# Performance work log

Measured on AMD Instinct MI355X. Metric: run time of the kernel, lower is better.

Reference implementation:

```python
import jax, jax.numpy as jnp
import numpy as np

B, T, C, H = 1, 2048, 1024, 16
HD = C // H           # 64
TOPK = 64
RAMP = 32
MAX_SPAN = 2048
NEG_MAX = jnp.finfo(jnp.float32).max


def setup_inputs() -> dict:
    key = jax.random.key(0)
    k0, k1, k2, k3, k4 = jax.random.split(key, 5)
    x = jax.random.normal(k0, (B, T, C), jnp.float32)
    w_attn = jax.random.normal(k1, (3 * C, C), jnp.float32) * 0.02
    w_proj = jax.random.normal(k2, (C, C), jnp.float32) * 0.02
    w_gate = jax.random.normal(k3, (C, C), jnp.float32) * 0.02
    span_params = jax.random.uniform(k4, (H,), jnp.float32)
    pos = jnp.arange(T, dtype=jnp.int64) if jax.config.jax_enable_x64 else jnp.arange(T, dtype=jnp.int32)
    return {"x": x, "w_attn": w_attn, "w_proj": w_proj, "w_gate": w_gate,
            "span_params": span_params, "pos": pos}


def _rotate_half(u):
    u1, u2 = jnp.split(u, 2, axis=-1)
    return jnp.concatenate([-u2, u1], axis=-1)


def _rope(q, k):
    t = q.shape[-2]
    inv_freq = 1.0 / (10000.0 ** (jnp.arange(0, HD, 2, dtype=jnp.float32) / HD))
    freqs = jnp.arange(t, dtype=jnp.float32)[:, None] * inv_freq[None, :]  # [T, HD/2]
    emb = jnp.concatenate([freqs, freqs], axis=-1)                          # [T, HD]
    cos = jnp.cos(emb)[None, None]
    sin = jnp.sin(emb)[None, None]
    q = q * cos + _rotate_half(q * sin)
    k = k * cos + _rotate_half(k * sin)
    return q, k


def reference(x, w_attn, w_proj, w_gate, span_params, pos):
    qkv = x @ w_attn.T                                   # [B,T,3C]
    q, k, v = jnp.split(qkv, 3, axis=-1)
    q = q.reshape(B, T, H, HD).transpose(0, 2, 1, 3)     # [B,H,T,HD]
    k = k.reshape(B, T, H, HD).transpose(0, 2, 1, 3)
    v = v.reshape(B, T, H, HD).transpose(0, 2, 1, 3)
    q, k = _rope(q, k)

    att = jnp.einsum('bhqd,bhkd->bhqk', q, k) / jnp.sqrt(jnp.float32(HD))
    i = jnp.arange(T)
    causal = i[:, None] >= i[None, :]                    # [T,T]
    att = jnp.where(causal[None, None], att, -jnp.inf)

    # sparse top-k with straight-through softmax
    top_vals = jax.lax.top_k(att, TOPK)[0]               # [B,H,T,K]
    thresh = top_vals[..., -1:]
    keep = (att >= thresh) & (att > -NEG_MAX)
    att_topk = jnp.where(keep, att, -NEG_MAX)
    topk_attn = jax.nn.softmax(att_topk, axis=-1)
    soft_attn = jax.nn.softmax(att, axis=-1)
    att = jax.lax.stop_gradient(topk_attn) + soft_attn - jax.lax.stop_gradient(soft_attn)

    # adaptive span soft mask + renormalize
    spans = MAX_SPAN * jnp.clip(span_params, 0.0, 1.0)   # [H]
    dist = jnp.abs(i[:, None] - i[None, :]).astype(jnp.float32)  # [T,T]
    soft_mask = jnp.clip((RAMP + spans[:, None, None] - dist[None]) / RAMP, 0.0, 1.0)  # [H,T,T]
    att = att * soft_mask[None]
    att = att / (att.sum(-1, keepdims=True) + 1e-8)

    y = jnp.einsum('bhqk,bhkd->bhqd', att, v)            # [B,H,T,HD]
    y = y.transpose(0, 2, 1, 3).reshape(B, T, C)
    gate = jax.nn.silu(x @ w_gate.T)
    y = y * gate
    y = y @ w_proj.T
    return y
```

## Files before the change

kernel.cpp:

```cpp
#include <hip/hip_runtime.h>
#include <math.h>

#define T_DIM 2048
#define C_DIM 1024
#define H_DIM 16
#define HD 64
#define TOPK_K 64
#define QTILE 8
#define LCAP 128

typedef __attribute__((ext_vector_type(8))) __bf16 bf16x8;
typedef __attribute__((ext_vector_type(4))) float f32x4;

__device__ __forceinline__ unsigned short bf16rn(float x) {
  unsigned u = __float_as_uint(x);
  return (unsigned short)((u + 0x7FFFu + ((u >> 16) & 1u)) >> 16);
}
__device__ __forceinline__ unsigned f2u(float f) {
  unsigned u = __float_as_uint(f);
  return (u & 0x80000000u) ? ~u : (u | 0x80000000u);
}
__device__ __forceinline__ float u2f(unsigned u) {
  unsigned v = (u & 0x80000000u) ? (u & 0x7FFFFFFFu) : ~u;
  return __uint_as_float(v);
}
__device__ __forceinline__ bf16x8 ld_frag(const uint4* p) {
  uint4 u = *p;
  return __builtin_bit_cast(bf16x8, u);
}
#define PAD_KEY 0x007FFFFFu

__global__ __launch_bounds__(256) void convert_all_kernel(
    const float* __restrict__ x, const float* __restrict__ wa,
    const float* __restrict__ wg, const float* __restrict__ wp,
    unsigned short* __restrict__ xh, unsigned short* __restrict__ xl,
    unsigned short* __restrict__ wqgh, unsigned short* __restrict__ wqgl,
    unsigned short* __restrict__ wph, unsigned short* __restrict__ wpl,
    float2* __restrict__ tab)
{
  const int tid = blockIdx.x * 256 + threadIdx.x;
  const int k8 = tid & 127, r = tid >> 7;
  if (r >= 7168) {
    const int e = ((r - 7168) << 7) | k8;
    const int t = e >> 5, d = e & 31;
    double invf = exp(-(double)d * (log(10000.0) / 32.0));
    double ang = (double)t * invf;
    tab[e] = make_float2((float)cos(ang), (float)sin(ang));
    return;
  }
  const float* src;
  unsigned short *Dh, *Dl;
  int srow, drow;
  if (r < 2048)      { src = x;  Dh = xh;   Dl = xl;   srow = r;        drow = r; }
  else if (r < 5120) { src = wa; Dh = wqgh; Dl = wqgl; srow = r - 2048; drow = r - 2048; }
  else if (r < 6144) { src = wg; Dh = wqgh; Dl = wqgl; srow = r - 5120; drow = r - 2048; }
  else               { src = wp; Dh = wph;  Dl = wpl;  srow = r - 6144; drow = r - 6144; }
  const float* s = src + ((size_t)srow << 10) + (k8 << 3);
  float4 a = *(const float4*)s;
  float4 b = *(const float4*)(s + 4);
  float xs[8] = {a.x, a.y, a.z, a.w, b.x, b.y, b.z, b.w};
  unsigned hi[8], lo[8];
#pragma unroll
  for (int jj = 0; jj < 8; ++jj) {
    unsigned short hb = bf16rn(xs[jj]);
    hi[jj] = hb;
    lo[jj] = bf16rn(xs[jj] - __uint_as_float((unsigned)hb << 16));
  }
  const int t16 = drow >> 4, rr = drow & 15, kc = k8 >> 2, kq = k8 & 3;
  const size_t elem = (((size_t)(t16 * 32 + kc)) * 64 + ((kq << 4) | rr)) * 8;
  uint4 vh, vl;
  vh.x = hi[0] | (hi[1] << 16); vh.y = hi[2] | (hi[3] << 16);
  vh.z = hi[4] | (hi[5] << 16); vh.w = hi[6] | (hi[7] << 16);
  vl.x = lo[0] | (lo[1] << 16); vl.y = lo[2] | (lo[3] << 16);
  vl.z = lo[4] | (lo[5] << 16); vl.w = lo[6] | (lo[7] << 16);
  *(uint4*)(Dh + elem) = vh;
  *(uint4*)(Dl + elem) = vl;
}

__device__ __forceinline__ void gld_lds16(const unsigned short* g, unsigned short* l) {
  __builtin_amdgcn_global_load_lds(
      (const __attribute__((address_space(1))) unsigned int*)g,
      (__attribute__((address_space(3))) unsigned int*)l, 16, 0, 0);
}

__global__ __launch_bounds__(512, 4) void mgemm_qkvg_kernel(
    const unsigned short* __restrict__ Ah, const unsigned short* __restrict__ Al,
    const unsigned short* __restrict__ Bh, const unsigned short* __restrict__ Bl,
    float* __restrict__ Cq, float* __restrict__ Ck, float* __restrict__ Cv,
    float* __restrict__ Cg)
{
  __shared__ __align__(16) unsigned short As[2 * 8 * 512];
  __shared__ __align__(16) unsigned short Bs[2 * 8 * 512];
  const int tid = threadIdx.x, lane = tid & 63, w = tid >> 6;
  const int mt0 = blockIdx.y << 3;
  const int nt0 = blockIdx.x << 3;

  f32x4 acc[8];
#pragma unroll
  for (int j = 0; j < 8; ++j) acc[j] = (f32x4){0.f, 0.f, 0.f, 0.f};

  for (int kc = 0; kc < 32; ++kc) {
#pragma unroll
    for (int li = 0; li < 4; ++li) {
      const int gi = (w << 2) + li;
      const int isB = gi >= 16;
      const int gb = gi & 15;
      const int t  = gb & 7;
      const int hl = gb >> 3;
      const unsigned short* gbase = isB ? (hl ? Bl : Bh) : (hl ? Al : Ah);
      const int tg = (isB ? nt0 : mt0) + t;
      const unsigned short* g = gbase + (((size_t)(tg * 32 + kc) << 6) + lane) * 8;
      unsigned short* l = (isB ? Bs : As) + hl * 4096 + t * 512;
      gld_lds16(g, l);
    }
    __syncthreads();
    bf16x8 ah = *(const bf16x8*)&As[w * 512 + lane * 8];
    bf16x8 al = *(const bf16x8*)&As[4096 + w * 512 + lane * 8];
#pragma unroll
    for (int j = 0; j < 8; ++j) {
      bf16x8 bh = *(const bf16x8*)&Bs[j * 512 + lane * 8];
      bf16x8 bl = *(const bf16x8*)&Bs[4096 + j * 512 + lane * 8];
      acc[j] = __builtin_amdgcn_mfma_f32_16x16x32_bf16(ah, bh, acc[j], 0, 0, 0);
      acc[j] = __builtin_amdgcn_mfma_f32_16x16x32_bf16(ah, bl, acc[j], 0, 0, 0);
      acc[j] = __builtin_amdgcn_mfma_f32_16x16x32_bf16(al, bh, acc[j], 0, 0, 0);
    }
    __syncthreads();
  }

  const int col = lane & 15, quad = lane >> 4;
  const int mbase = (blockIdx.y << 7) + (w << 4);
#pragma unroll
  for (int j = 0; j < 8; ++j) {
    const int ncol = (blockIdx.x << 7) + (j << 4);
    const int which = ncol >> 10;
    if (which < 3) {
      const int h = (ncol & 1023) >> 6;
      float* dst = (which == 0) ? Cq : (which == 1) ? Ck : Cv;
      float* base = dst + (((size_t)h * T_DIM) << 6) + (ncol & 63) + col;
#pragma unroll
      for (int reg = 0; reg < 4; ++reg) {
        const int m = mbase + quad * 4 + reg;
        base[(size_t)m << 6] = acc[j][reg];
      }
    } else {
      const int cb = (ncol & 1023) + col;
#pragma unroll
      for (int reg = 0; reg < 4; ++reg) {
        const int m = mbase + quad * 4 + reg;
        float vv = acc[j][reg];
        Cg[((size_t)m << 10) + cb] = vv / (1.f + expf(-vv));
      }
    }
  }
}

__global__ __launch_bounds__(256, 4) void mgemm_proj_kernel(
    const unsigned short* __restrict__ Ah, const unsigned short* __restrict__ Al,
    const unsigned short* __restrict__ Bh, const unsigned short* __restrict__ Bl,
    float* __restrict__ P0, float* __restrict__ P1)
{
  __shared__ __align__(16) unsigned short As[2 * 4 * 512];
  __shared__ __align__(16) unsigned short Bs[2 * 8 * 512];
  const int tid = threadIdx.x, lane = tid & 63, w = tid >> 6;
  const int mt0 = blockIdx.y << 2;
  const int nt0 = blockIdx.x << 3;
  const int kc0 = blockIdx.z << 4;
  float* Cout = blockIdx.z ? P1 : P0;

  f32x4 acc[8];
#pragma unroll
  for (int j = 0; j < 8; ++j) acc[j] = (f32x4){0.f, 0.f, 0.f, 0.f};

  for (int kc = kc0; kc < kc0 + 16; ++kc) {
#pragma unroll
    for (int li = 0; li < 6; ++li) {
      const int gi = w * 6 + li;
      const int isB = gi >= 8;
      const int t  = isB ? ((gi - 8) & 7) : (gi & 3);
      const int hl = isB ? ((gi - 8) >> 3) : (gi >> 2);
      const unsigned short* gbase = isB ? (hl ? Bl : Bh) : (hl ? Al : Ah);
      const int tg = (isB ? nt0 : mt0) + t;
      const unsigned short* g = gbase + (((size_t)(tg * 32 + kc) << 6) + lane) * 8;
      unsigned short* l = isB ? (Bs + hl * 4096 + t * 512) : (As + hl * 2048 + t * 512);
      gld_lds16(g, l);
    }
    __syncthreads();
    bf16x8 ah = *(const bf16x8*)&As[w * 512 + lane * 8];
    bf16x8 al = *(const bf16x8*)&As[2048 + w * 512 + lane * 8];
#pragma unroll
    for (int j = 0; j < 8; ++j) {
      bf16x8 bh = *(const bf16x8*)&Bs[j * 512 + lane * 8];
      bf16x8 bl = *(const bf16x8*)&Bs[4096 + j * 512 + lane * 8];
      acc[j] = __builtin_amdgcn_mfma_f32_16x16x32_bf16(ah, bh, acc[j], 0, 0, 0);
      acc[j] = __builtin_amdgcn_mfma_f32_16x16x32_bf16(ah, bl, acc[j], 0, 0, 0);
      acc[j] = __builtin_amdgcn_mfma_f32_16x16x32_bf16(al, bh, acc[j], 0, 0, 0);
    }
    __syncthreads();
  }

  const int col = lane & 15, quad = lane >> 4;
  const int mbase = (blockIdx.y << 6) + (w << 4);
  const int nbase = blockIdx.x << 7;
#pragma unroll
  for (int j = 0; j < 8; ++j)
#pragma unroll
    for (int reg = 0; reg < 4; ++reg) {
      const int m = mbase + quad * 4 + reg;
      Cout[((size_t)m << 10) + nbase + (j << 4) + col] = acc[j][reg];
    }
}

__global__ __launch_bounds__(256) void add2_kernel(
    const float* __restrict__ P0, const float* __restrict__ P1,
    float* __restrict__ out)
{
  const int i = (blockIdx.x * 256 + threadIdx.x) << 2;
  float4 a = *(const float4*)(P0 + i);
  float4 b = *(const float4*)(P1 + i);
  float4 o = {a.x + b.x, a.y + b.y, a.z + b.z, a.w + b.w};
  *(float4*)(out + i) = o;
}

__global__ __launch_bounds__(64) void prep_frag_kernel(
    float* __restrict__ qb, float* __restrict__ kb,
    const float2* __restrict__ tab)
{
  float* buf = blockIdx.z ? kb : qb;
  const int lane = threadIdx.x;
  const int t16 = blockIdx.x, h = blockIdx.y;
  const int nr = lane & 15, quad = lane >> 4;
  const int t = (t16 << 4) + nr;
  const float* row = buf + ((size_t)(h * T_DIM + t) << 6);
  const int d0 = quad << 3;
  float4 a0 = *(const float4*)(row + d0);
  float4 a1 = *(const float4*)(row + d0 + 4);
  float4 b0 = *(const float4*)(row + 32 + d0);
  float4 b1 = *(const float4*)(row + 32 + d0 + 4);
  float x0[8] = {a0.x, a0.y, a0.z, a0.w, a1.x, a1.y, a1.z, a1.w};
  float x1[8] = {b0.x, b0.y, b0.z, b0.w, b1.x, b1.y, b1.z, b1.w};
  const float2* tb = tab + t * 32 + d0;
  unsigned short h0[8], l0[8], h1[8], l1[8];
#pragma unroll
  for (int jj = 0; jj < 8; ++jj) {
    float2 cs2 = tb[jj];
    float o0 = fmaf(x0[jj], cs2.x, -x1[jj] * cs2.y);
    float o1 = fmaf(x1[jj], cs2.x, x0[jj] * cs2.y);
    unsigned short hb = bf16rn(o0);
    h0[jj] = hb;
    l0[jj] = bf16rn(o0 - __uint_as_float((unsigned)hb << 16));
    hb = bf16rn(o1);
    h1[jj] = hb;
    l1[jj] = bf16rn(o1 - __uint_as_float((unsigned)hb << 16));
  }
  char* base = (char*)buf + (((size_t)(h * 128 + t16)) << 12);
  uint4 v;
  v.x = (unsigned)h0[0] | ((unsigned)h0[1] << 16);
  v.y = (unsigned)h0[2] | ((unsigned)h0[3] << 16);
  v.z = (unsigned)h0[4] | ((unsigned)h0[5] << 16);
  v.w = (unsigned)h0[6] | ((unsigned)h0[7] << 16);
  ((uint4*)base)[lane] = v;
  v.x = (unsigned)h1[0] | ((unsigned)h1[1] << 16);
  v.y = (unsigned)h1[2] | ((unsigned)h1[3] << 16);
  v.z = (unsigned)h1[4] | ((unsigned)h1[5] << 16);
  v.w = (unsigned)h1[6] | ((unsigned)h1[7] << 16);
  ((uint4*)(base + 1024))[lane] = v;
  v.x = (unsigned)l0[0] | ((unsigned)l0[1] << 16);
  v.y = (unsigned)l0[2] | ((unsigned)l0[3] << 16);
  v.z = (unsigned)l0[4] | ((unsigned)l0[5] << 16);
  v.w = (unsigned)l0[6] | ((unsigned)l0[7] << 16);
  ((uint4*)(base + 2048))[lane] = v;
  v.x = (unsigned)l1[0] | ((unsigned)l1[1] << 16);
  v.y = (unsigned)l1[2] | ((unsigned)l1[3] << 16);
  v.z = (unsigned)l1[4] | ((unsigned)l1[5] << 16);
  v.w = (unsigned)l1[6] | ((unsigned)l1[7] << 16);
  ((uint4*)(base + 3072))[lane] = v;
}

__global__ __launch_bounds__(512, 6) void attn_kernel(
    const float* __restrict__ qfrag, const float* __restrict__ kfrag,
    const float* __restrict__ v, const float* __restrict__ span_params,
    const float* __restrict__ gate,
    unsigned short* __restrict__ Yh, unsigned short* __restrict__ Yl)
{
  __shared__ __align__(16) char smem[QTILE * 1024 * 4];
  float* sBase = (float*)smem;
  unsigned* histB = (unsigned*)smem;
  int* listJB = (int*)(smem + 8192);
  unsigned* listUB = (unsigned*)(smem + 12288);

  const int tid = threadIdx.x;
  const int lane = tid & 63;
  const int w = tid >> 6;
  const int bx = gridDim.x - 1 - blockIdx.x;
  const int q0 = bx << 3;
  const int h = blockIdx.y;
  const int qi = q0 + w;
  const int n = qi + 1;
  const float* vh = v + (((size_t)h * T_DIM) << 6);
  const int col = lane & 15, quad = lane >> 4;

  const int qt16 = bx >> 1;
  const int rlo = (bx & 1) << 3;
  const uint4* qf = (const uint4*)((const char*)qfrag + (((size_t)(h * 128 + qt16)) << 12));
  bf16x8 Ah0 = ld_frag(qf + lane);
  bf16x8 Ah1 = ld_frag(qf + 64 + lane);
  bf16x8 Al0 = ld_frag(qf + 128 + lane);
  bf16x8 Al1 = ld_frag(qf + 192 + lane);

  unsigned uk[32];

#pragma unroll
  for (int ph = 0; ph < 2; ++ph) {
    const int tlo = ph << 6;
    const int thi = (qt16 < tlo + 63) ? qt16 : (tlo + 63);
    int tf = tlo + w;
    if (tf <= thi) {
      const uint4* kf = (const uint4*)((const char*)kfrag + (((size_t)(h * 128 + tf)) << 12));
      bf16x8 nBh0 = ld_frag(kf + lane);
      bf16x8 nBh1 = ld_frag(kf + 64 + lane);
      bf16x8 nBl0 = ld_frag(kf + 128 + lane);
      bf16x8 nBl1 = ld_frag(kf + 192 + lane);
      for (; tf <= thi; tf += 8) {
        const bf16x8 Bh0 = nBh0, Bh1 = nBh1, Bl0 = nBl0, Bl1 = nBl1;
        const int tn = (tf + 8 <= thi) ? (tf + 8) : tf;
        const uint4* kfn = (const uint4*)((const char*)kfrag + (((size_t)(h * 128 + tn)) << 12));
        nBh0 = ld_frag(kfn + lane);
        nBh1 = ld_frag(kfn + 64 + lane);
        nBl0 = ld_frag(kfn + 128 + lane);
        nBl1 = ld_frag(kfn + 192 + lane);
        f32x4 acc = {0.f, 0.f, 0.f, 0.f};
        acc = __builtin_amdgcn_mfma_f32_16x16x32_bf16(Ah0, Bh0, acc, 0, 0, 0);
        acc = __builtin_amdgcn_mfma_f32_16x16x32_bf16(Ah0, Bl0, acc, 0, 0, 0);
        acc = __builtin_amdgcn_mfma_f32_16x16x32_bf16(Al0, Bh0, acc, 0, 0, 0);
        acc = __builtin_amdgcn_mfma_f32_16x16x32_bf16(Ah1, Bh1, acc, 0, 0, 0);
        acc = __builtin_amdgcn_mfma_f32_16x16x32_bf16(Ah1, Bl1, acc, 0, 0, 0);
        acc = __builtin_amdgcn_mfma_f32_16x16x32_bf16(Al1, Bh1, acc, 0, 0, 0);
        const int jcol = (tf << 4) + col;
#pragma unroll
        for (int r = 0; r < 4; ++r) {
          const int row8 = (quad << 2) + r - rlo;
          if ((unsigned)row8 < 8u && jcol <= q0 + row8)
            sBase[row8 * 1024 + ((jcol & 1023) ^ (((row8 >> 2) & 1) << 4))] = acc[r];
        }
      }
    }
    __syncthreads();
#pragma unroll
    for (int cc = 0; cc < 2; ++cc) {
      const int c = (ph << 1) + cc;
      if ((c << 9) < n) {
#pragma unroll
        for (int i = 0; i < 8; ++i) {
          const int j = (((c << 3) + i) << 6) + lane;
          uk[(c << 3) + i] = (j < n)
              ? f2u(sBase[w * 1024 + ((j & 1023) ^ (((w >> 2) & 1) << 4))]) : PAD_KEY;
        }
      } else {
#pragma unroll
        for (int i = 0; i < 8; ++i) uk[(c << 3) + i] = PAD_KEY;
      }
    }
    __syncthreads();
  }

  unsigned* hist = histB + (w << 8);
  int* listJ = listJB + (w << 7);
  unsigned* listU = listUB + (w << 7);
  const float span = 2048.f * fminf(fmaxf(span_params[h], 0.f), 1.f);

  unsigned umax = 0;
#pragma unroll
  for (int i = 0; i < 32; ++i) umax = max(umax, uk[i]);
#pragma unroll
  for (int off = 32; off > 0; off >>= 1)
    umax = max(umax, (unsigned)__shfl_xor((int)umax, off, 64));
  const float mraw = u2f(umax);

  unsigned thresh_u = 0;
  if (n > TOPK_K) {
    unsigned want = TOPK_K;
    const unsigned bmax = umax >> 24;
    unsigned long long c01 = 0;
#pragma unroll
    for (int c = 0; c < 4; ++c) {
      if ((c << 9) < n) {
#pragma unroll
        for (int i = 0; i < 8; ++i) {
          const unsigned u = uk[(c << 3) + i];
          const unsigned d = bmax - (u >> 24);
          if (u > PAD_KEY && d < 4u) c01 += 1ull << (d << 4);
        }
      }
    }
#pragma unroll
    for (int off = 32; off > 0; off >>= 1)
      c01 += __shfl_xor(c01, off, 64);
    unsigned cnt8[8];
    cnt8[0] = (unsigned)c01 & 0xFFFFu;
    cnt8[1] = ((unsigned)c01) >> 16;
    cnt8[2] = (unsigned)(c01 >> 32) & 0xFFFFu;
    cnt8[3] = (unsigned)(c01 >> 48);
    int m = -1;
    unsigned cumBefore = 0;
    bool exact = false;
    unsigned cum = 0;
#pragma unroll
    for (int b = 0; b < 4; ++b) {
      if (m < 0 && cum + cnt8[b] >= want) {
        m = b; cumBefore = cum; exact = (cum + cnt8[b] == want);
      }
      cum += cnt8[b];
    }
    if (m < 0) {
      unsigned long long c23 = 0;
#pragma unroll
      for (int c = 0; c < 4; ++c) {
        if ((c << 9) < n) {
#pragma unroll
          for (int i = 0; i < 8; ++i) {
            const unsigned u = uk[(c << 3) + i];
            const unsigned d = bmax - (u >> 24) - 4u;
            if (u > PAD_KEY && d < 4u) c23 += 1ull << (d << 4);
          }
        }
      }
#pragma unroll
      for (int off = 32; off > 0; off >>= 1)
        c23 += __shfl_xor(c23, off, 64);
      cnt8[4] = (unsigned)c23 & 0xFFFFu;
      cnt8[5] = ((unsigned)c23) >> 16;
      cnt8[6] = (unsigned)(c23 >> 32) & 0xFFFFu;
      cnt8[7] = (unsigned)(c23 >> 48);
#pragma unroll
      for (int b = 4; b < 8; ++b) {
        if (m < 0 && cum + cnt8[b] >= want) {
          m = b; cumBefore = cum; exact = (cum + cnt8[b] == want);
        }
        cum += cnt8[b];
      }
    }
    unsigned prefix;
    int shift0;
    if (m >= 0) { prefix = (bmax - (unsigned)m) << 24; want -= cumBefore; shift0 = 16; }
    else        { prefix = 0; shift0 = 24; }
    if (m >= 0 && exact) {
      thresh_u = prefix;
    } else {
      for (int shift = shift0; shift >= 0; shift -= 8) {
        uint4 z4 = {0u, 0u, 0u, 0u};
        *(uint4*)&hist[lane << 2] = z4;
        __threadfence_block();
        const unsigned pm = (shift == 24) ? 0u : (0xFFFFFFFFu << (shift + 8));
#pragma unroll
        for (int c = 0; c < 4; ++c) {
          if ((c << 9) < n) {
#pragma unroll
            for (int i = 0; i < 8; ++i) {
              const unsigned u = uk[(c << 3) + i];
              if (u > PAD_KEY && (u & pm) == prefix)
                atomicAdd(&hist[(u >> shift) & 255u], 1u);
            }
          }
        }
        __threadfence_block();
        uint4 hv = *(const uint4*)&hist[lane << 2];
        unsigned loc = hv.x + hv.y + hv.z + hv.w;
        unsigned suf = loc;
#pragma unroll
        for (int off = 1; off < 64; off <<= 1) {
          unsigned t = __shfl_down(suf, off, 64);
          suf += (lane + off < 64) ? t : 0u;
        }
        unsigned sufE = suf - loc;
        unsigned S3 = sufE + hv.w;
        unsigned S2 = S3 + hv.z;
        unsigned S1 = S2 + hv.y;
        unsigned S0 = S1 + hv.x;
        const unsigned wt = want;
        int found = 0;
        unsigned pk = 0;
        if (S0 >= wt && S1 < wt)
          { found = 1; pk = ((unsigned)(4*lane+0) << 16) | ((S0 == wt) ? 0x8000u : 0u) | (wt - S1); }
        if (S1 >= wt && S2 < wt)
          { found = 1; pk = ((unsigned)(4*lane+1) << 16) | ((S1 == wt) ? 0x8000u : 0u) | (wt - S2); }
        if (S2 >= wt && S3 < wt)
          { found = 1; pk = ((unsigned)(4*lane+2) << 16) | ((S2 == wt) ? 0x8000u : 0u) | (wt - S3); }
        if (S3 >= wt && sufE < wt)
          { found = 1; pk = ((unsigned)(4*lane+3) << 16) | ((S3 == wt) ? 0x8000u : 0u) | (wt - sufE); }
        unsigned long long mk = __ballot(found);
        int src = __ffsll(mk) - 1;
        pk = __shfl(pk, src, 64);
        prefix |= (pk >> 16) << shift;
        want = pk & 0x7FFFu;
        if (pk & 0x8000u) break;
      }
      thresh_u = prefix;
    }
  }

  int cnt_run = 0;
#pragma unroll
  for (int c = 0; c < 4; ++c) {
    if ((c << 9) < n) {
#pragma unroll
      for (int i = 0; i < 8; ++i) {
        const int j = (((c << 3) + i) << 6) + lane;
        const unsigned u = uk[(c << 3) + i];
        const bool keep = (u >= thresh_u) && (u > PAD_KEY);
        unsigned long long mb = __ballot(keep);
        if (keep) {
          int pos = cnt_run + (int)__popcll(mb & ((1ull << lane) - 1ull));
          if (pos < LCAP) { listJ[pos] = j; listU[pos] = u; }
        }
        cnt_run += (int)__popcll(mb);
      }
    }
  }
  const int cnt = min(cnt_run, LCAP);
  __threadfence_block();

  float Zl = 0.f, Ul = 0.f;
  for (int e = lane; e < cnt; e += 64) {
    const unsigned u = listU[e];
    const int j = listJ[e];
    const float wv = __expf((u2f(u) - mraw) * 0.125f);
    const float dist = (float)(qi - j);
    const float msk = fminf(fmaxf((32.f + span - dist) * (1.f / 32.f), 0.f), 1.f);
    const float wm = wv * msk;
    Zl += wv;
    Ul += wm;
    listU[e] = __float_as_uint(wm);
  }
#pragma unroll
  for (int off = 32; off > 0; off >>= 1) {
    Zl += __shfl_xor(Zl, off, 64);
    Ul += __shfl_xor(Ul, off, 64);
  }
  const float scale = 1.f / (Ul + 1e-8f * Zl);
  __threadfence_block();

  const int g = lane >> 4;
  const int d4 = col << 2;
  float4 acc4 = {0.f, 0.f, 0.f, 0.f};
  for (int e0 = 0; e0 < cnt; e0 += 16) {
    int j0 = 0, j1 = 0, j2 = 0, j3 = 0;
    float wm0 = 0.f, wm1 = 0.f, wm2 = 0.f, wm3 = 0.f;
    {
      const int e = e0 + g;
      if (e < cnt) { j0 = listJ[e]; wm0 = __uint_as_float(listU[e]); }
    }
    {
      const int e = e0 + 4 + g;
      if (e < cnt) { j1 = listJ[e]; wm1 = __uint_as_float(listU[e]); }
    }
    {
      const int e = e0 + 8 + g;
      if (e < cnt) { j2 = listJ[e]; wm2 = __uint_as_float(listU[e]); }
    }
    {
      const int e = e0 + 12 + g;
      if (e < cnt) { j3 = listJ[e]; wm3 = __uint_as_float(listU[e]); }
    }
    const float4 v0 = *(const float4*)(vh + ((size_t)j0 << 6) + d4);
    const float4 v1 = *(const float4*)(vh + ((size_t)j1 << 6) + d4);
    const float4 v2 = *(const float4*)(vh + ((size_t)j2 << 6) + d4);
    const float4 v3 = *(const float4*)(vh + ((size_t)j3 << 6) + d4);
    acc4.x = fmaf(wm0, v0.x, acc4.x);
    acc4.y = fmaf(wm0, v0.y, acc4.y);
    acc4.z = fmaf(wm0, v0.z, acc4.z);
    acc4.w = fmaf(wm0, v0.w, acc4.w);
    acc4.x = fmaf(wm1, v1.x, acc4.x);
    acc4.y = fmaf(wm1, v1.y, acc4.y);
    acc4.z = fmaf(wm1, v1.z, acc4.z);
    acc4.w = fmaf(wm1, v1.w, acc4.w);
    acc4.x = fmaf(wm2, v2.x, acc4.x);
    acc4.y = fmaf(wm2, v2.y, acc4.y);
    acc4.z = fmaf(wm2, v2.z, acc4.z);
    acc4.w = fmaf(wm2, v2.w, acc4.w);
    acc4.x = fmaf(wm3, v3.x, acc4.x);
    acc4.y = fmaf(wm3, v3.y, acc4.y);
    acc4.z = fmaf(wm3, v3.z, acc4.z);
    acc4.w = fmaf(wm3, v3.w, acc4.w);
  }
#pragma unroll
  for (int off = 16; off <= 32; off <<= 1) {
    acc4.x += __shfl_xor(acc4.x, off, 64);
    acc4.y += __shfl_xor(acc4.y, off, 64);
    acc4.z += __shfl_xor(acc4.z, off, 64);
    acc4.w += __shfl_xor(acc4.w, off, 64);
  }
  if (g == 0) {
    const int c0 = (h << 6) + d4;
    const float4 gv = *(const float4*)(gate + ((size_t)qi << 10) + c0);
    float p[4] = {acc4.x * scale * gv.x, acc4.y * scale * gv.y,
                  acc4.z * scale * gv.z, acc4.w * scale * gv.w};
    unsigned short ph[4], pl[4];
#pragma unroll
    for (int jj = 0; jj < 4; ++jj) {
      unsigned short hb = bf16rn(p[jj]);
      ph[jj] = hb;
      pl[jj] = bf16rn(p[jj] - __uint_as_float((unsigned)hb << 16));
    }
    const int k8 = c0 >> 3;
    const int t16 = qi >> 4, rr = qi & 15, kc = k8 >> 2, kq = k8 & 3;
    const size_t elem = (((size_t)(t16 * 32 + kc)) * 64 + ((kq << 4) | rr)) * 8 + (d4 & 7);
    ushort4 vh4 = {ph[0], ph[1], ph[2], ph[3]};
    ushort4 vl4 = {pl[0], pl[1], pl[2], pl[3]};
    *(ushort4*)(Yh + elem) = vh4;
    *(ushort4*)(Yl + elem) = vl4;
  }
}

extern "C" void kernel_launch(void* const* d_in, const int* in_sizes, int n_in,
                              void* d_out, int out_size, void* d_ws, size_t ws_size,
                              hipStream_t stream) {
  (void)in_sizes; (void)n_in; (void)out_size; (void)ws_size;
  const float* x           = (const float*)d_in[0];
  const float* w_attn      = (const float*)d_in[1];
  const float* w_proj      = (const float*)d_in[2];
  const float* w_gate      = (const float*)d_in[3];
  const float* span_params = (const float*)d_in[4];
  float* out = (float*)d_out;

  char* ws = (char*)d_ws;
  const size_t MB = 1024 * 1024;
  float* q     = (float*)(ws);
  float* k     = (float*)(ws + 8 * MB);
  float* v     = (float*)(ws + 16 * MB);
  float* gate  = (float*)(ws + 24 * MB);
  unsigned short* xf_h  = (unsigned short*)(ws + 40 * MB);
  unsigned short* xf_l  = (unsigned short*)(ws + 44 * MB);
  unsigned short* wqg_h = (unsigned short*)(ws + 48 * MB);
  unsigned short* wqg_l = (unsigned short*)(ws + 56 * MB);
  unsigned short* wfp_h = (unsigned short*)(ws + 64 * MB);
  unsigned short* wfp_l = (unsigned short*)(ws + 66 * MB);
  unsigned short* ygf_h = (unsigned short*)(ws + 68 * MB);
  unsigned short* ygf_l = (unsigned short*)(ws + 72 * MB);
  float2* rope_tab = (float2*)(ws + 76 * MB);
  float* P0 = q;
  float* P1 = k;

  convert_all_kernel<<<3840, 256, 0, stream>>>(
      x, w_attn, w_gate, w_proj, xf_h, xf_l, wqg_h, wqg_l, wfp_h, wfp_l, rope_tab);
  mgemm_qkvg_kernel<<<dim3(32, 16), 512, 0, stream>>>(
      xf_h, xf_l, wqg_h, wqg_l, q, k, v, gate);
  prep_frag_kernel<<<dim3(T_DIM / 16, H_DIM, 2), 64, 0, stream>>>(q, k, rope_tab);
  attn_kernel<<<dim3(T_DIM / QTILE, H_DIM), 512, 0, stream>>>(
      q, k, v, span_params, gate, ygf_h, ygf_l);
  mgemm_proj_kernel<<<dim3(8, 32, 2), 256, 0, stream>>>(
      ygf_h, ygf_l, wfp_h, wfp_l, P0, P1);
  add2_kernel<<<(T_DIM * C_DIM) / 1024, 256, 0, stream>>>(P0, P1, out);
}
```

Before: 281.2 us.

## Fuse RoPE fragment prep into QKV GEMM epilogue and split proj GEMM 4-way

The RoPE rotation and bf16 hi/lo fragment packing for Q and K now run in the QKV GEMM epilogue, staged through LDS, which removes the separate prep_frag kernel and its extra fp32 round trip through global memory. The output projection GEMM is split four ways along K instead of two, doubling the block count for better CU occupancy. That costs more partial-sum traffic in a four-input reduction kernel and a larger LDS footprint in the QKV GEMM.

```diff
diff --git a/kernel.cpp b/kernel.cpp
--- a/kernel.cpp
+++ b/kernel.cpp
@@ -87,10 +87,11 @@
     const unsigned short* __restrict__ Ah, const unsigned short* __restrict__ Al,
     const unsigned short* __restrict__ Bh, const unsigned short* __restrict__ Bl,
     float* __restrict__ Cq, float* __restrict__ Ck, float* __restrict__ Cv,
-    float* __restrict__ Cg)
+    float* __restrict__ Cg, const float2* __restrict__ tab)
 {
-  __shared__ __align__(16) unsigned short As[2 * 8 * 512];
-  __shared__ __align__(16) unsigned short Bs[2 * 8 * 512];
+  __shared__ __align__(16) char smemAll[34816];
+  unsigned short* As = (unsigned short*)smemAll;
+  unsigned short* Bs = (unsigned short*)(smemAll + 16384);
   const int tid = threadIdx.x, lane = tid & 63, w = tid >> 6;
   const int mt0 = blockIdx.y << 3;
   const int nt0 = blockIdx.x << 3;
@@ -128,27 +129,85 @@
   }
 
   const int col = lane & 15, quad = lane >> 4;
-  const int mbase = (blockIdx.y << 7) + (w << 4);
-#pragma unroll
-  for (int j = 0; j < 8; ++j) {
-    const int ncol = (blockIdx.x << 7) + (j << 4);
-    const int which = ncol >> 10;
-    if (which < 3) {
-      const int h = (ncol & 1023) >> 6;
-      float* dst = (which == 0) ? Cq : (which == 1) ? Ck : Cv;
-      float* base = dst + (((size_t)h * T_DIM) << 6) + (ncol & 63) + col;
-#pragma unroll
-      for (int reg = 0; reg < 4; ++reg) {
-        const int m = mbase + quad * 4 + reg;
-        base[(size_t)m << 6] = acc[j][reg];
-      }
-    } else {
-      const int cb = (ncol & 1023) + col;
-#pragma unroll
-      for (int reg = 0; reg < 4; ++reg) {
-        const int m = mbase + quad * 4 + reg;
-        float vv = acc[j][reg];
-        Cg[((size_t)m << 10) + cb] = vv / (1.f + expf(-vv));
+  const int bxx = blockIdx.x;
+  if (bxx < 16) {
+    float* W = (float*)smemAll + w * (16 * 66);
+    float* qkbuf = (bxx < 8) ? Cq : Ck;
+    const int hb = (bxx & 7) << 1;
+    const int t16 = (blockIdx.y << 3) + w;
+    const int t = (t16 << 4) + col;
+    const float2* tb = tab + t * 32 + (quad << 3);
+#pragma unroll
+    for (int jh = 0; jh < 2; ++jh) {
+#pragma unroll
+      for (int j2 = 0; j2 < 4; ++j2)
+#pragma unroll
+        for (int reg = 0; reg < 4; ++reg)
+          W[(quad * 4 + reg) * 66 + (j2 << 4) + col] = acc[(jh << 2) + j2][reg];
+      const float* rowp = W + col * 66;
+      float x0[8], x1[8];
+#pragma unroll
+      for (int jj = 0; jj < 8; ++jj) {
+        x0[jj] = rowp[(quad << 3) + jj];
+        x1[jj] = rowp[32 + (quad << 3) + jj];
+      }
+      unsigned short h0[8], l0[8], h1[8], l1[8];
+#pragma unroll
+      for (int jj = 0; jj < 8; ++jj) {
+        float2 cs2 = tb[jj];
+        float o0 = fmaf(x0[jj], cs2.x, -x1[jj] * cs2.y);
+        float o1 = fmaf(x1[jj], cs2.x, x0[jj] * cs2.y);
+        unsigned short hbb = bf16rn(o0);
+        h0[jj] = hbb;
+        l0[jj] = bf16rn(o0 - __uint_as_float((unsigned)hbb << 16));
+        hbb = bf16rn(o1);
+        h1[jj] = hbb;
+        l1[jj] = bf16rn(o1 - __uint_as_float((unsigned)hbb << 16));
+      }
+      char* base = (char*)qkbuf + (((size_t)((hb + jh) * 128 + t16)) << 12);
+      uint4 v;
+      v.x = (unsigned)h0[0] | ((unsigned)h0[1] << 16);
+      v.y = (unsigned)h0[2] | ((unsigned)h0[3] << 16);
+      v.z = (unsigned)h0[4] | ((unsigned)h0[5] << 16);
+      v.w = (unsigned)h0[6] | ((unsigned)h0[7] << 16);
+      ((uint4*)base)[lane] = v;
+      v.x = (unsigned)h1[0] | ((unsigned)h1[1] << 16);
+      v.y = (unsigned)h1[2] | ((unsigned)h1[3] << 16);
+      v.z = (unsigned)h1[4] | ((unsigned)h1[5] << 16);
+      v.w = (unsigned)h1[6] | ((unsigned)h1[7] << 16);
+      ((uint4*)(base + 1024))[lane] = v;
+      v.x = (unsigned)l0[0] | ((unsigned)l0[1] << 16);
+      v.y = (unsigned)l0[2] | ((unsigned)l0[3] << 16);
+      v.z = (unsigned)l0[4] | ((unsigned)l0[5] << 16);
+      v.w = (unsigned)l0[6] | ((unsigned)l0[7] << 16);
+      ((uint4*)(base + 2048))[lane] = v;
+      v.x = (unsigned)l1[0] | ((unsigned)l1[1] << 16);
+      v.y = (unsigned)l1[2] | ((unsigned)l1[3] << 16);
+      v.z = (unsigned)l1[4] | ((unsigned)l1[5] << 16);
+      v.w = (unsigned)l1[6] | ((unsigned)l1[7] << 16);
+      ((uint4*)(base + 3072))[lane] = v;
+    }
+  } else {
+    const int mbase = (blockIdx.y << 7) + (w << 4);
+#pragma unroll
+    for (int j = 0; j < 8; ++j) {
+      const int ncol = (bxx << 7) + (j << 4);
+      if (bxx < 24) {
+        const int h = (ncol & 1023) >> 6;
+        float* base = Cv + (((size_t)h * T_DIM) << 6) + (ncol & 63) + col;
+#pragma unroll
+        for (int reg = 0; reg < 4; ++reg) {
+          const int m = mbase + quad * 4 + reg;
+          base[(size_t)m << 6] = acc[j][reg];
+        }
+      } else {
+        const int cb = (ncol & 1023) + col;
+#pragma unroll
+        for (int reg = 0; reg < 4; ++reg) {
+          const int m = mbase + quad * 4 + reg;
+          float vv = acc[j][reg];
+          Cg[((size_t)m << 10) + cb] = vv / (1.f + expf(-vv));
+        }
       }
     }
   }
@@ -157,21 +216,23 @@
 __global__ __launch_bounds__(256, 4) void mgemm_proj_kernel(
     const unsigned short* __restrict__ Ah, const unsigned short* __restrict__ Al,
     const unsigned short* __restrict__ Bh, const unsigned short* __restrict__ Bl,
-    float* __restrict__ P0, float* __restrict__ P1)
+    float* __restrict__ P0, float* __restrict__ P1,
+    float* __restrict__ P2, float* __restrict__ P3)
 {
   __shared__ __align__(16) unsigned short As[2 * 4 * 512];
   __shared__ __align__(16) unsigned short Bs[2 * 8 * 512];
   const int tid = threadIdx.x, lane = tid & 63, w = tid >> 6;
   const int mt0 = blockIdx.y << 2;
   const int nt0 = blockIdx.x << 3;
-  const int kc0 = blockIdx.z << 4;
-  float* Cout = blockIdx.z ? P1 : P0;
+  const int kc0 = blockIdx.z << 3;
+  float* Cout = (blockIdx.z == 0) ? P0 : (blockIdx.z == 1) ? P1
+              : (blockIdx.z == 2) ? P2 : P3;
 
   f32x4 acc[8];
 #pragma unroll
   for (int j = 0; j < 8; ++j) acc[j] = (f32x4){0.f, 0.f, 0.f, 0.f};
 
-  for (int kc = kc0; kc < kc0 + 16; ++kc) {
+  for (int kc = kc0; kc < kc0 + 8; ++kc) {
 #pragma unroll
     for (int li = 0; li < 6; ++li) {
       const int gi = w * 6 + li;
@@ -210,70 +271,19 @@
     }
 }
 
-__global__ __launch_bounds__(256) void add2_kernel(
+__global__ __launch_bounds__(256) void add4_kernel(
     const float* __restrict__ P0, const float* __restrict__ P1,
+    const float* __restrict__ P2, const float* __restrict__ P3,
     float* __restrict__ out)
 {
   const int i = (blockIdx.x * 256 + threadIdx.x) << 2;
   float4 a = *(const float4*)(P0 + i);
   float4 b = *(const float4*)(P1 + i);
-  float4 o = {a.x + b.x, a.y + b.y, a.z + b.z, a.w + b.w};
+  float4 c = *(const float4*)(P2 + i);
+  float4 d = *(const float4*)(P3 + i);
+  float4 o = {a.x + b.x + c.x + d.x, a.y + b.y + c.y + d.y,
+              a.z + b.z + c.z + d.z, a.w + b.w + c.w + d.w};
   *(float4*)(out + i) = o;
-}
-
-__global__ __launch_bounds__(64) void prep_frag_kernel(
-    float* __restrict__ qb, float* __restrict__ kb,
-    const float2* __restrict__ tab)
-{
-  float* buf = blockIdx.z ? kb : qb;
-  const int lane = threadIdx.x;
-  const int t16 = blockIdx.x, h = blockIdx.y;
-  const int nr = lane & 15, quad = lane >> 4;
-  const int t = (t16 << 4) + nr;
-  const float* row = buf + ((size_t)(h * T_DIM + t) << 6);
-  const int d0 = quad << 3;
-  float4 a0 = *(const float4*)(row + d0);
-  float4 a1 = *(const float4*)(row + d0 + 4);
-  float4 b0 = *(const float4*)(row + 32 + d0);
-  float4 b1 = *(const float4*)(row + 32 + d0 + 4);
-  float x0[8] = {a0.x, a0.y, a0.z, a0.w, a1.x, a1.y, a1.z, a1.w};
-  float x1[8] = {b0.x, b0.y, b0.z, b0.w, b1.x, b1.y, b1.z, b1.w};
-  const float2* tb = tab + t * 32 + d0;
-  unsigned short h0[8], l0[8], h1[8], l1[8];
-#pragma unroll
-  for (int jj = 0; jj < 8; ++jj) {
-    float2 cs2 = tb[jj];
-    float o0 = fmaf(x0[jj], cs2.x, -x1[jj] * cs2.y);
-    float o1 = fmaf(x1[jj], cs2.x, x0[jj] * cs2.y);
-    unsigned short hb = bf16rn(o0);
-    h0[jj] = hb;
-    l0[jj] = bf16rn(o0 - __uint_as_float((unsigned)hb << 16));
-    hb = bf16rn(o1);
-    h1[jj] = hb;
-    l1[jj] = bf16rn(o1 - __uint_as_float((unsigned)hb << 16));
-  }
-  char* base = (char*)buf + (((size_t)(h * 128 + t16)) << 12);
-  uint4 v;
-  v.x = (unsigned)h0[0] | ((unsigned)h0[1] << 16);
-  v.y = (unsigned)h0[2] | ((unsigned)h0[3] << 16);
-  v.z = (unsigned)h0[4] | ((unsigned)h0[5] << 16);
-  v.w = (unsigned)h0[6] | ((unsigned)h0[7] << 16);
-  ((uint4*)base)[lane] = v;
-  v.x = (unsigned)h1[0] | ((unsigned)h1[1] << 16);
-  v.y = (unsigned)h1[2] | ((unsigned)h1[3] << 16);
-  v.z = (unsigned)h1[4] | ((unsigned)h1[5] << 16);
-  v.w = (unsigned)h1[6] | ((unsigned)h1[7] << 16);
-  ((uint4*)(base + 1024))[lane] = v;
-  v.x = (unsigned)l0[0] | ((unsigned)l0[1] << 16);
-  v.y = (unsigned)l0[2] | ((unsigned)l0[3] << 16);
-  v.z = (unsigned)l0[4] | ((unsigned)l0[5] << 16);
-  v.w = (unsigned)l0[6] | ((unsigned)l0[7] << 16);
-  ((uint4*)(base + 2048))[lane] = v;
-  v.x = (unsigned)l1[0] | ((unsigned)l1[1] << 16);
-  v.y = (unsigned)l1[2] | ((unsigned)l1[3] << 16);
-  v.z = (unsigned)l1[4] | ((unsigned)l1[5] << 16);
-  v.w = (unsigned)l1[6] | ((unsigned)l1[7] << 16);
-  ((uint4*)(base + 3072))[lane] = v;
 }
 
 __global__ __launch_bounds__(512, 6) void attn_kernel(
@@ -628,6 +638,7 @@
   float* k     = (float*)(ws + 8 * MB);
   float* v     = (float*)(ws + 16 * MB);
   float* gate  = (float*)(ws + 24 * MB);
+  float* P2    = (float*)(ws + 32 * MB);
   unsigned short* xf_h  = (unsigned short*)(ws + 40 * MB);
   unsigned short* xf_l  = (unsigned short*)(ws + 44 * MB);
   unsigned short* wqg_h = (unsigned short*)(ws + 48 * MB);
@@ -639,15 +650,15 @@
   float2* rope_tab = (float2*)(ws + 76 * MB);
   float* P0 = q;
   float* P1 = k;
+  float* P3 = gate;
 
   convert_all_kernel<<<3840, 256, 0, stream>>>(
       x, w_attn, w_gate, w_proj, xf_h, xf_l, wqg_h, wqg_l, wfp_h, wfp_l, rope_tab);
   mgemm_qkvg_kernel<<<dim3(32, 16), 512, 0, stream>>>(
-      xf_h, xf_l, wqg_h, wqg_l, q, k, v, gate);
-  prep_frag_kernel<<<dim3(T_DIM / 16, H_DIM, 2), 64, 0, stream>>>(q, k, rope_tab);
+      xf_h, xf_l, wqg_h, wqg_l, q, k, v, gate, rope_tab);
   attn_kernel<<<dim3(T_DIM / QTILE, H_DIM), 512, 0, stream>>>(
       q, k, v, span_params, gate, ygf_h, ygf_l);
-  mgemm_proj_kernel<<<dim3(8, 32, 2), 256, 0, stream>>>(
-      ygf_h, ygf_l, wfp_h, wfp_l, P0, P1);
-  add2_kernel<<<(T_DIM * C_DIM) / 1024, 256, 0, stream>>>(P0, P1, out);
-}
+  mgemm_proj_kernel<<<dim3(8, 32, 4), 256, 0, stream>>>(
+      ygf_h, ygf_l, wfp_h, wfp_l, P0, P1, P2, P3);
+  add4_kernel<<<(T_DIM * C_DIM) / 1024, 256, 0, stream>>>(P0, P1, P2, P3, out);
+}
```

Result: no change. 285.0 us (+1.3%).
